# Performance work log

Hardware: AMD Instinct MI355X
Metric: run time of the kernel (lower is better)

Reference implementation:

```python
import jax, jax.numpy as jnp
import numpy as np


def _rope(v, pos, head_dim):
    # v: [H, D]; rotate consecutive pairs by angle pos * theta_j
    theta = 1.0 / (10000.0 ** (jnp.arange(0, head_dim, 2, dtype=jnp.float32) / head_dim))
    ang = pos * theta                      # [D/2]
    cos, sin = jnp.cos(ang), jnp.sin(ang)
    vr = v.reshape(v.shape[0], -1, 2)      # [H, D/2, 2]
    re = vr[..., 0] * cos - vr[..., 1] * sin
    im = vr[..., 0] * sin + vr[..., 1] * cos
    return jnp.stack([re, im], axis=-1).reshape(v.shape)


def setup_inputs() -> dict:
    key = jax.random.key(0)
    ks = jax.random.split(key, 7)
    dim, H, D, S = 4096, 32, 128, 2048
    scale = 0.02
    return {
        "x": jax.random.normal(ks[0], (dim,), dtype=jnp.float32),
        "wq": jax.random.normal(ks[1], (dim, dim), dtype=jnp.float32) * scale,
        "wk": jax.random.normal(ks[2], (dim, dim), dtype=jnp.float32) * scale,
        "wv": jax.random.normal(ks[3], (dim, dim), dtype=jnp.float32) * scale,
        "wo": jax.random.normal(ks[4], (dim, dim), dtype=jnp.float32) * scale,
        "cache_k": jax.random.normal(ks[5], (S, H, D), dtype=jnp.float32),
        "cache_v": jax.random.normal(ks[6], (S, H, D), dtype=jnp.float32),
        "pos": 1536,
    }


def reference(x, wq, wk, wv, wo, cache_k, cache_v, pos):
    H, D = cache_k.shape[1], cache_k.shape[2]
    # nn.Linear without bias: y = W @ x
    xq = (wq @ x).reshape(H, D)
    xk = (wk @ x).reshape(H, D)
    xv = (wv @ x).reshape(H, D)
    xq = _rope(xq, pos, D)
    xk = _rope(xk, pos, D)
    # KV cache append (pos is a static Python int)
    cache_k = cache_k.at[pos].set(xk)
    cache_v = cache_v.at[pos].set(xv)
    keys = cache_k[: pos + 1]              # [P, H, D]
    values = cache_v[: pos + 1]            # [P, H, D]
    # single-query decode attention per head
    scores = jnp.einsum("hd,phd->hp", xq, keys) / jnp.sqrt(jnp.float32(D))
    scores = jax.nn.softmax(scores, axis=-1)
    out = jnp.einsum("hp,phd->hd", scores, values)   # [H, D]
    return wo @ out.reshape(-1)
```

## Files before the change

### kernel.cpp

```cpp
#include <hip/hip_runtime.h>
#include <math.h>

#define DIM 4096
#define H 32
#define D 128
#define SMAX 2048
#define CHUNK 32
#define NCHUNK (SMAX / CHUNK)
#define PART_STRIDE 130

__global__ void matvec_qkv(const float* __restrict__ wq, const float* __restrict__ wk,
                           const float* __restrict__ wv, const float* __restrict__ x,
                           float* __restrict__ y) {
    int row  = blockIdx.x * 4 + (threadIdx.x >> 6);
    int lane = threadIdx.x & 63;
    const float* w;
    if (row < DIM)            w = wq + (size_t)row * DIM;
    else if (row < 2 * DIM)   w = wk + (size_t)(row - DIM) * DIM;
    else                      w = wv + (size_t)(row - 2 * DIM) * DIM;

    float a0 = 0.f, a1 = 0.f, a2 = 0.f, a3 = 0.f;
#pragma unroll
    for (int i = 0; i < DIM / (64 * 4); ++i) {
        int idx = (i * 64 + lane) * 4;
        const float4 a = *reinterpret_cast<const float4*>(w + idx);
        const float4 b = *reinterpret_cast<const float4*>(x + idx);
        a0 = fmaf(a.x, b.x, a0);
        a1 = fmaf(a.y, b.y, a1);
        a2 = fmaf(a.z, b.z, a2);
        a3 = fmaf(a.w, b.w, a3);
    }
    float acc = (a0 + a1) + (a2 + a3);
#pragma unroll
    for (int off = 32; off; off >>= 1) acc += __shfl_xor(acc, off);
    if (lane == 0) y[row] = acc;
}

__global__ void matvec_o(const float* __restrict__ w_, const float* __restrict__ v,
                         float* __restrict__ y) {
    int row  = blockIdx.x * 4 + (threadIdx.x >> 6);
    int lane = threadIdx.x & 63;
    const float* w = w_ + (size_t)row * DIM;
    float a0 = 0.f, a1 = 0.f, a2 = 0.f, a3 = 0.f;
#pragma unroll
    for (int i = 0; i < DIM / (64 * 4); ++i) {
        int idx = (i * 64 + lane) * 4;
        const float4 a = *reinterpret_cast<const float4*>(w + idx);
        const float4 b = *reinterpret_cast<const float4*>(v + idx);
        a0 = fmaf(a.x, b.x, a0);
        a1 = fmaf(a.y, b.y, a1);
        a2 = fmaf(a.z, b.z, a2);
        a3 = fmaf(a.w, b.w, a3);
    }
    float acc = (a0 + a1) + (a2 + a3);
#pragma unroll
    for (int off = 32; off; off >>= 1) acc += __shfl_xor(acc, off);
    if (lane == 0) y[row] = acc;
}

__global__ void rope_qk(float* __restrict__ xq, float* __restrict__ xk,
                        const int* __restrict__ pos_p) {
    int tid = blockIdx.x * blockDim.x + threadIdx.x;
    if (tid >= 2 * H * (D / 2)) return;
    int pos = *pos_p;
    float* base = (tid < H * (D / 2)) ? xq : xk;
    int r = tid & (H * (D / 2) - 1);
    int h = r >> 6;
    int j = r & 63;
    float theta = powf(10000.0f, -(float)(2 * j) / (float)D);
    float ang = (float)pos * theta;
    float s, c;
    sincosf(ang, &s, &c);
    float* v = base + h * D + 2 * j;
    float v0 = v[0], v1 = v[1];
    v[0] = v0 * c - v1 * s;
    v[1] = v0 * s + v1 * c;
}

__global__ void attn_partial(const float* __restrict__ cache_k, const float* __restrict__ cache_v,
                             const float* __restrict__ xq, const float* __restrict__ xk,
                             const float* __restrict__ xv, const int* __restrict__ pos_p,
                             float* __restrict__ partials) {
    __shared__ float lds_m[4], lds_l[4];
    __shared__ float lds_acc[4][128];
    int h = blockIdx.x;
    int c = blockIdx.y;
    int lane = threadIdx.x;
    int g  = lane >> 4;
    int gl = lane & 15;
    int pos = *pos_p;
    int base = c * CHUNK;
    int p1 = min(base + CHUNK, pos + 1);
    float* pp = partials + (size_t)(h * NCHUNK + c) * PART_STRIDE;

    if (base > pos) {
        if (lane == 0) { pp[0] = -INFINITY; pp[1] = 0.f; }
        reinterpret_cast<float2*>(pp + 2)[lane] = make_float2(0.f, 0.f);
        return;
    }

    const float4* qv = reinterpret_cast<const float4*>(xq + h * D + gl * 8);
    const float4 q0 = qv[0], q1 = qv[1];

    float m = -INFINITY, l = 0.f;
    float4 acc0 = make_float4(0.f, 0.f, 0.f, 0.f);
    float4 acc1 = make_float4(0.f, 0.f, 0.f, 0.f);

    for (int p = base + g; p < p1; p += 4) {
        const float* kp = (p == pos) ? (xk + h * D)
                                     : (cache_k + ((size_t)p * H + h) * D);
        const float4* kv4 = reinterpret_cast<const float4*>(kp + gl * 8);
        float4 k0 = kv4[0], k1 = kv4[1];
        float d = q0.x * k0.x + q0.y * k0.y + q0.z * k0.z + q0.w * k0.w
                + q1.x * k1.x + q1.y * k1.y + q1.z * k1.z + q1.w * k1.w;
        d += __shfl_xor(d, 1);
        d += __shfl_xor(d, 2);
        d += __shfl_xor(d, 4);
        d += __shfl_xor(d, 8);
        float s = d * 0.08838834764831845f;
        float mn = fmaxf(m, s);
        float corr = __expf(m - mn);
        float wgt  = __expf(s - mn);
        const float* vp = (p == pos) ? (xv + h * D)
                                     : (cache_v + ((size_t)p * H + h) * D);
        const float4* vv4 = reinterpret_cast<const float4*>(vp + gl * 8);
        float4 v0 = vv4[0], v1 = vv4[1];
        l = l * corr + wgt;
        acc0.x = fmaf(wgt, v0.x, acc0.x * corr);
        acc0.y = fmaf(wgt, v0.y, acc0.y * corr);
        acc0.z = fmaf(wgt, v0.z, acc0.z * corr);
        acc0.w = fmaf(wgt, v0.w, acc0.w * corr);
        acc1.x = fmaf(wgt, v1.x, acc1.x * corr);
        acc1.y = fmaf(wgt, v1.y, acc1.y * corr);
        acc1.z = fmaf(wgt, v1.z, acc1.z * corr);
        acc1.w = fmaf(wgt, v1.w, acc1.w * corr);
        m = mn;
    }

    if (gl == 0) { lds_m[g] = m; lds_l[g] = l; }
    *reinterpret_cast<float4*>(&lds_acc[g][gl * 8])     = acc0;
    *reinterpret_cast<float4*>(&lds_acc[g][gl * 8 + 4]) = acc1;
    __syncthreads();
    float M = fmaxf(fmaxf(lds_m[0], lds_m[1]), fmaxf(lds_m[2], lds_m[3]));
    float w0 = __expf(lds_m[0] - M);
    float w1 = __expf(lds_m[1] - M);
    float w2 = __expf(lds_m[2] - M);
    float w3 = __expf(lds_m[3] - M);
    float L  = w0 * lds_l[0] + w1 * lds_l[1] + w2 * lds_l[2] + w3 * lds_l[3];
    int d0 = 2 * lane;
    float s0 = w0 * lds_acc[0][d0]     + w1 * lds_acc[1][d0]
             + w2 * lds_acc[2][d0]     + w3 * lds_acc[3][d0];
    float s1 = w0 * lds_acc[0][d0 + 1] + w1 * lds_acc[1][d0 + 1]
             + w2 * lds_acc[2][d0 + 1] + w3 * lds_acc[3][d0 + 1];
    if (lane == 0) { pp[0] = M; pp[1] = L; }
    reinterpret_cast<float2*>(pp + 2)[lane] = make_float2(s0, s1);
}

__global__ void attn_combine(const float* __restrict__ partials, float* __restrict__ out_attn) {
    int h = blockIdx.x;
    int lane = threadIdx.x;
    float m = -INFINITY;
    for (int c = 0; c < NCHUNK; ++c)
        m = fmaxf(m, partials[(size_t)(h * NCHUNK + c) * PART_STRIDE]);
    float L = 0.f, a0 = 0.f, a1 = 0.f;
    for (int c = 0; c < NCHUNK; ++c) {
        const float* pp = partials + (size_t)(h * NCHUNK + c) * PART_STRIDE;
        float w = __expf(pp[0] - m);
        L += pp[1] * w;
        float2 a = reinterpret_cast<const float2*>(pp + 2)[lane];
        a0 += w * a.x;
        a1 += w * a.y;
    }
    float inv = 1.f / L;
    out_attn[h * D + 2 * lane]     = a0 * inv;
    out_attn[h * D + 2 * lane + 1] = a1 * inv;
}

extern "C" void kernel_launch(void* const* d_in, const int* in_sizes, int n_in,
                              void* d_out, int out_size, void* d_ws, size_t ws_size,
                              hipStream_t stream) {
    const float* x       = (const float*)d_in[0];
    const float* wq      = (const float*)d_in[1];
    const float* wk      = (const float*)d_in[2];
    const float* wv      = (const float*)d_in[3];
    const float* wo      = (const float*)d_in[4];
    const float* cache_k = (const float*)d_in[5];
    const float* cache_v = (const float*)d_in[6];
    const int*   pos     = (const int*)d_in[7];

    float* ws       = (float*)d_ws;
    float* xq       = ws;
    float* xk       = ws + DIM;
    float* xv       = ws + 2 * DIM;
    float* partials = ws + 3 * DIM;
    float* out_attn = partials + H * NCHUNK * PART_STRIDE;
    float* out      = (float*)d_out;

    matvec_qkv<<<3 * DIM / 4, 256, 0, stream>>>(wq, wk, wv, x, ws);
    rope_qk<<<16, 256, 0, stream>>>(xq, xk, pos);
    attn_partial<<<dim3(H, NCHUNK), 64, 0, stream>>>(cache_k, cache_v, xq, xk, xv, pos, partials);
    attn_combine<<<H, 64, 0, stream>>>(partials, out_attn);
    matvec_o<<<DIM / 4, 256, 0, stream>>>(wo, out_attn, out);
}
```

Before: 82.28 us.

## Fuse QKV matvec with RoPE and software-pipeline weight loads in matvecs

Merges the QKV projection and RoPE into one kernel. Each wave computes an adjacent row pair for q, k and v and applies the rotation directly in registers, which removes a kernel launch and a global round trip. Both matvecs now keep x in registers and double-buffer weight loads in half-row chunks, with scheduling barriers to keep loads in flight. Each wave handles two rows instead of one, so the grid is smaller and register pressure is higher.

Result: no change. 82.72 us (+0.5%).

```diff
diff --git a/kernel.cpp b/kernel.cpp
--- a/kernel.cpp
+++ b/kernel.cpp
@@ -9,72 +9,130 @@
 #define NCHUNK (SMAX / CHUNK)
 #define PART_STRIDE 130
 
-__global__ void matvec_qkv(const float* __restrict__ wq, const float* __restrict__ wk,
-                           const float* __restrict__ wv, const float* __restrict__ x,
-                           float* __restrict__ y) {
-    int row  = blockIdx.x * 4 + (threadIdx.x >> 6);
-    int lane = threadIdx.x & 63;
-    const float* w;
-    if (row < DIM)            w = wq + (size_t)row * DIM;
-    else if (row < 2 * DIM)   w = wk + (size_t)(row - DIM) * DIM;
-    else                      w = wv + (size_t)(row - 2 * DIM) * DIM;
-
-    float a0 = 0.f, a1 = 0.f, a2 = 0.f, a3 = 0.f;
-#pragma unroll
-    for (int i = 0; i < DIM / (64 * 4); ++i) {
-        int idx = (i * 64 + lane) * 4;
-        const float4 a = *reinterpret_cast<const float4*>(w + idx);
-        const float4 b = *reinterpret_cast<const float4*>(x + idx);
-        a0 = fmaf(a.x, b.x, a0);
-        a1 = fmaf(a.y, b.y, a1);
-        a2 = fmaf(a.z, b.z, a2);
-        a3 = fmaf(a.w, b.w, a3);
-    }
-    float acc = (a0 + a1) + (a2 + a3);
-#pragma unroll
-    for (int off = 32; off; off >>= 1) acc += __shfl_xor(acc, off);
-    if (lane == 0) y[row] = acc;
-}
-
-__global__ void matvec_o(const float* __restrict__ w_, const float* __restrict__ v,
-                         float* __restrict__ y) {
-    int row  = blockIdx.x * 4 + (threadIdx.x >> 6);
-    int lane = threadIdx.x & 63;
-    const float* w = w_ + (size_t)row * DIM;
-    float a0 = 0.f, a1 = 0.f, a2 = 0.f, a3 = 0.f;
-#pragma unroll
-    for (int i = 0; i < DIM / (64 * 4); ++i) {
-        int idx = (i * 64 + lane) * 4;
-        const float4 a = *reinterpret_cast<const float4*>(w + idx);
-        const float4 b = *reinterpret_cast<const float4*>(v + idx);
-        a0 = fmaf(a.x, b.x, a0);
-        a1 = fmaf(a.y, b.y, a1);
-        a2 = fmaf(a.z, b.z, a2);
-        a3 = fmaf(a.w, b.w, a3);
-    }
-    float acc = (a0 + a1) + (a2 + a3);
-#pragma unroll
-    for (int off = 32; off; off >>= 1) acc += __shfl_xor(acc, off);
-    if (lane == 0) y[row] = acc;
-}
-
-__global__ void rope_qk(float* __restrict__ xq, float* __restrict__ xk,
-                        const int* __restrict__ pos_p) {
-    int tid = blockIdx.x * blockDim.x + threadIdx.x;
-    if (tid >= 2 * H * (D / 2)) return;
-    int pos = *pos_p;
-    float* base = (tid < H * (D / 2)) ? xq : xk;
-    int r = tid & (H * (D / 2) - 1);
-    int h = r >> 6;
-    int j = r & 63;
-    float theta = powf(10000.0f, -(float)(2 * j) / (float)D);
-    float ang = (float)pos * theta;
-    float s, c;
-    sincosf(ang, &s, &c);
-    float* v = base + h * D + 2 * j;
-    float v0 = v[0], v1 = v[1];
-    v[0] = v0 * c - v1 * s;
-    v[1] = v0 * s + v1 * c;
+typedef float v4f __attribute__((ext_vector_type(4)));
+
+__device__ __forceinline__ void load_half(v4f (&buf)[8], const float* __restrict__ wp, int off) {
+#pragma unroll
+    for (int i = 0; i < 8; ++i)
+        buf[i] = *reinterpret_cast<const v4f*>(wp + i * 256 + off);
+}
+
+template <int XO>
+__device__ __forceinline__ float dot_half(const v4f (&buf)[8], const v4f (&xr)[16]) {
+    float s0 = 0.f, s1 = 0.f, s2 = 0.f, s3 = 0.f;
+#pragma unroll
+    for (int i = 0; i < 8; ++i) {
+        s0 = fmaf(buf[i].x, xr[XO + i].x, s0);
+        s1 = fmaf(buf[i].y, xr[XO + i].y, s1);
+        s2 = fmaf(buf[i].z, xr[XO + i].z, s2);
+        s3 = fmaf(buf[i].w, xr[XO + i].w, s3);
+    }
+    return (s0 + s1) + (s2 + s3);
+}
+
+__device__ __forceinline__ float wave_sum(float v) {
+#pragma unroll
+    for (int o = 32; o; o >>= 1) v += __shfl_xor(v, o);
+    return v;
+}
+
+#define SB() __builtin_amdgcn_sched_barrier(0)
+
+__global__ void __launch_bounds__(256) qkv_rope(
+        const float* __restrict__ wq, const float* __restrict__ wk,
+        const float* __restrict__ wv, const float* __restrict__ x,
+        const int* __restrict__ pos_p,
+        float* __restrict__ xq, float* __restrict__ xk, float* __restrict__ xv) {
+    int t = threadIdx.x, lane = t & 63;
+    int W = blockIdx.x * 4 + (t >> 6);
+    int r0 = W * 2;
+    int off = lane * 4;
+
+    v4f xr[16];
+#pragma unroll
+    for (int i = 0; i < 16; ++i)
+        xr[i] = *reinterpret_cast<const v4f*>(x + i * 256 + off);
+
+    const float* q0 = wq + (size_t)r0 * DIM;
+    const float* k0 = wk + (size_t)r0 * DIM;
+    const float* v0 = wv + (size_t)r0 * DIM;
+
+    v4f A[8], B[8];
+    float dq0, dq1, dk0, dk1, dv0, dv1;
+
+    load_half(A, q0, off);
+    load_half(B, q0 + 2048, off);            SB();
+    dq0  = dot_half<0>(A, xr);
+    load_half(A, q0 + DIM, off);             SB();
+    dq0 += dot_half<8>(B, xr);
+    load_half(B, q0 + DIM + 2048, off);      SB();
+    dq1  = dot_half<0>(A, xr);
+    load_half(A, k0, off);                   SB();
+    dq1 += dot_half<8>(B, xr);
+    load_half(B, k0 + 2048, off);            SB();
+    dk0  = dot_half<0>(A, xr);
+    load_half(A, k0 + DIM, off);             SB();
+    dk0 += dot_half<8>(B, xr);
+    load_half(B, k0 + DIM + 2048, off);      SB();
+    dk1  = dot_half<0>(A, xr);
+    load_half(A, v0, off);                   SB();
+    dk1 += dot_half<8>(B, xr);
+    load_half(B, v0 + 2048, off);            SB();
+    dv0  = dot_half<0>(A, xr);
+    load_half(A, v0 + DIM, off);             SB();
+    dv0 += dot_half<8>(B, xr);
+    load_half(B, v0 + DIM + 2048, off);      SB();
+    dv1  = dot_half<0>(A, xr);
+    dv1 += dot_half<8>(B, xr);
+
+    dq0 = wave_sum(dq0); dq1 = wave_sum(dq1);
+    dk0 = wave_sum(dk0); dk1 = wave_sum(dk1);
+    dv0 = wave_sum(dv0); dv1 = wave_sum(dv1);
+
+    if (lane == 0) {
+        int pos = *pos_p;
+        int j = W & 63;
+        float theta = powf(10000.0f, -(float)(2 * j) / (float)D);
+        float ang = (float)pos * theta;
+        float s, c;
+        sincosf(ang, &s, &c);
+        xq[r0]     = dq0 * c - dq1 * s;
+        xq[r0 + 1] = dq0 * s + dq1 * c;
+        xk[r0]     = dk0 * c - dk1 * s;
+        xk[r0 + 1] = dk0 * s + dk1 * c;
+        xv[r0]     = dv0;
+        xv[r0 + 1] = dv1;
+    }
+}
+
+__global__ void __launch_bounds__(256) matvec_o(
+        const float* __restrict__ w_, const float* __restrict__ vin,
+        float* __restrict__ y) {
+    int t = threadIdx.x, lane = t & 63;
+    int W = blockIdx.x * 4 + (t >> 6);
+    int r0 = W * 2;
+    int off = lane * 4;
+
+    v4f xr[16];
+#pragma unroll
+    for (int i = 0; i < 16; ++i)
+        xr[i] = *reinterpret_cast<const v4f*>(vin + i * 256 + off);
+
+    const float* w0 = w_ + (size_t)r0 * DIM;
+
+    v4f A[8], B[8];
+    float d0, d1;
+    load_half(A, w0, off);
+    load_half(B, w0 + 2048, off);            SB();
+    d0  = dot_half<0>(A, xr);
+    load_half(A, w0 + DIM, off);             SB();
+    d0 += dot_half<8>(B, xr);
+    load_half(B, w0 + DIM + 2048, off);      SB();
+    d1  = dot_half<0>(A, xr);
+    d1 += dot_half<8>(B, xr);
+
+    d0 = wave_sum(d0); d1 = wave_sum(d1);
+    if (lane == 0) { y[r0] = d0; y[r0 + 1] = d1; }
 }
 
 __global__ void attn_partial(const float* __restrict__ cache_k, const float* __restrict__ cache_v,
@@ -196,9 +254,8 @@
     float* out_attn = partials + H * NCHUNK * PART_STRIDE;
     float* out      = (float*)d_out;
 
-    matvec_qkv<<<3 * DIM / 4, 256, 0, stream>>>(wq, wk, wv, x, ws);
-    rope_qk<<<16, 256, 0, stream>>>(xq, xk, pos);
+    qkv_rope<<<512, 256, 0, stream>>>(wq, wk, wv, x, pos, xq, xk, xv);
     attn_partial<<<dim3(H, NCHUNK), 64, 0, stream>>>(cache_k, cache_v, xq, xk, xv, pos, partials);
     attn_combine<<<H, 64, 0, stream>>>(partials, out_attn);
-    matvec_o<<<DIM / 4, 256, 0, stream>>>(wo, out_attn, out);
-}
+    matvec_o<<<512, 256, 0, stream>>>(wo, out_attn, out);
+}
```
